# Kernel optimization log

Hardware: AMD Instinct MI355X
Metric: run time of the kernel (lower is better)

## Reference

```python
import jax, jax.numpy as jnp
import numpy as np

N, E = 50000, 800000
IN_DIM, HID, ZDIM = 256, 128, 64
LN_EPS = 1e-5


def _layernorm(x, gamma, beta):
    mu = jnp.mean(x, axis=-1, keepdims=True)
    var = jnp.mean(jnp.square(x - mu), axis=-1, keepdims=True)
    return (x - mu) * jax.lax.rsqrt(var + LN_EPS) * gamma + beta


def _gcn_conv(h, src, dst, dinv, W, b):
    # h: (N, d_in) -> (N, d_out). GCNConv: X W, then sym-normalized
    # aggregation over edges with self-loops, then bias.
    h = h @ W                                   # (N, d_out)
    coef = dinv[src] * dinv[dst]                # (E,)
    agg = jax.ops.segment_sum(h[src] * coef[:, None], dst,
                              num_segments=h.shape[0])
    agg = agg + h * jnp.square(dinv)[:, None]   # self-loop term
    return agg + b


def setup_inputs() -> dict:
    key = jax.random.key(0)
    ks = jax.random.split(key, 5)
    x = jax.random.normal(ks[0], (N, IN_DIM), dtype=jnp.float32)
    edge_index = jax.random.randint(ks[1], (2, E), 0, N, dtype=jnp.int64)
    s1 = 1.0 / np.sqrt(IN_DIM)
    s2 = 1.0 / np.sqrt(HID)
    return {
        "x": x,
        "edge_index": edge_index,
        "ln_gamma": jnp.ones((IN_DIM,), jnp.float32),
        "ln_beta": jnp.zeros((IN_DIM,), jnp.float32),
        "W1": jax.random.normal(ks[2], (IN_DIM, HID), jnp.float32) * s1,
        "b1": jnp.zeros((HID,), jnp.float32),
        "W2": jax.random.normal(ks[3], (HID, HID), jnp.float32) * s2,
        "b2": jnp.zeros((HID,), jnp.float32),
        "W3": jax.random.normal(ks[4], (HID, ZDIM), jnp.float32) * s2,
        "b3": jnp.zeros((ZDIM,), jnp.float32),
    }


def reference(x, edge_index, ln_gamma, ln_beta, W1, b1, W2, b2, W3, b3):
    src, dst = edge_index[0], edge_index[1]
    n = x.shape[0]
    # degree with self-loops (dropout is inference no-op, training=False)
    deg = jnp.ones((n,), x.dtype).at[dst].add(1.0)
    dinv = jax.lax.rsqrt(deg)
    h = _layernorm(x, ln_gamma, ln_beta)
    h = jax.nn.relu(_gcn_conv(h, src, dst, dinv, W1, b1))
    h = jax.nn.relu(_gcn_conv(h, src, dst, dinv, W2, b2))
    z = _gcn_conv(h, src, dst, dinv, W3, b3)
    return z
```

## Files before the change

### kernel.cpp

```cpp
#include <hip/hip_runtime.h>
#include <cstdint>
#include <cstddef>


typedef __attribute__((ext_vector_type(8))) __bf16 bf16x8;
typedef __attribute__((ext_vector_type(4))) float f32x4;
typedef _Float16 half_t;
typedef __attribute__((ext_vector_type(8))) _Float16 half8_t;

#define NHIST 256
#define CHUNK 4096
#define MAXB 8192

__global__ __launch_bounds__(256) void prep_misc(
    const int* __restrict__ dst,
    const float* __restrict__ W1, const float* __restrict__ W2,
    const float* __restrict__ W3,
    int* __restrict__ bcnt_multi,
    unsigned short* __restrict__ W1t_hi, unsigned short* __restrict__ W1t_lo,
    unsigned short* __restrict__ W2t_hi, unsigned short* __restrict__ W2t_lo,
    unsigned short* __restrict__ W3t_hi, unsigned short* __restrict__ W3t_lo,
    int E) {
  int blk = blockIdx.x;
  int tid = threadIdx.x;
  if (blk < NHIST) {
    __shared__ int h[256];
    h[tid] = 0;
    __syncthreads();
    for (int e = blk * 256 + tid; e < E; e += NHIST * 256)
      atomicAdd(&h[dst[e] >> 8], 1);
    __syncthreads();
    bcnt_multi[blk * 256 + tid] = h[tid];
    return;
  }
  int idx = (blk - NHIST) * 256 + tid;
  if (idx < 32768) {
    int k = idx / 128, c = idx % 128;
    float v = W1[idx];
    __bf16 h = (__bf16)v;
    __bf16 l = (__bf16)(v - (float)h);
    W1t_hi[(size_t)c * 256 + k] = __builtin_bit_cast(unsigned short, h);
    W1t_lo[(size_t)c * 256 + k] = __builtin_bit_cast(unsigned short, l);
    return;
  }
  const float* W;
  unsigned short *Th, *Tl;
  int K, NOUT;
  if (idx < 49152) {
    idx -= 32768;
    W = W2; Th = W2t_hi; Tl = W2t_lo; K = 128; NOUT = 128;
  } else {
    idx -= 49152;
    W = W3; Th = W3t_hi; Tl = W3t_lo; K = 128; NOUT = 64;
  }
  int k = idx / NOUT, c = idx % NOUT;
  float v = W[idx];
  half_t h = (half_t)v;
  half_t l = (half_t)((v - (float)h) * 2048.0f);
  Th[(size_t)c * K + k] = __builtin_bit_cast(unsigned short, h);
  Tl[(size_t)c * K + k] = __builtin_bit_cast(unsigned short, l);
}

__global__ __launch_bounds__(256) void scan_buckets(const int* __restrict__ bcnt_multi,
                                                    int* __restrict__ bbase,
                                                    int* __restrict__ bcur, int NB, int E) {
  __shared__ int tmp[256];
  int t = threadIdx.x;
  int v = 0;
  for (int h = 0; h < NHIST; ++h) v += bcnt_multi[h * 256 + t];
  tmp[t] = v;
  __syncthreads();
  for (int off = 1; off < 256; off <<= 1) {
    int x = (t >= off) ? tmp[t - off] : 0;
    __syncthreads();
    tmp[t] += x;
    __syncthreads();
  }
  int excl = tmp[t] - v;
  if (t < NB) { bbase[t] = excl; bcur[t] = excl; }
  if (t == 0) bbase[NB] = E;
}

__device__ __forceinline__ void scatter_body(char* smem_raw, int bid,
                                             const int* __restrict__ src,
                                             const int* __restrict__ dst,
                                             int* __restrict__ bcur,
                                             unsigned int* __restrict__ binned, int E) {
  unsigned int* recs = (unsigned int*)smem_raw;
  int* hist = (int*)(smem_raw + 16384);
  int* lbase = hist + 256;
  int* resv = lbase + 256;
  int* cur = resv + 256;
  int t = threadIdx.x;
  int e0 = bid * CHUNK;
  if (e0 >= E) return;
  int len = min(CHUNK, E - e0);
  hist[t] = 0;
  cur[t] = 0;
  __syncthreads();
  for (int i = t; i < len; i += 256) atomicAdd(&hist[dst[e0 + i] >> 8], 1);
  __syncthreads();
  int v = hist[t];
  lbase[t] = v;
  __syncthreads();
  for (int off = 1; off < 256; off <<= 1) {
    int x = (t >= off) ? lbase[t - off] : 0;
    __syncthreads();
    lbase[t] += x;
    __syncthreads();
  }
  int myexcl = lbase[t] - v;
  if (v) resv[t] = atomicAdd(&bcur[t], v);
  __syncthreads();
  lbase[t] = myexcl;
  __syncthreads();
  for (int i = t; i < len; i += 256) {
    int d = dst[e0 + i], s = src[e0 + i];
    int b = d >> 8;
    int r = atomicAdd(&cur[b], 1);
    recs[lbase[b] + r] = ((unsigned int)d << 16) | (unsigned int)s;
  }
  __syncthreads();
  for (int i = t; i < len; i += 256) {
    unsigned int rc = recs[i];
    int b = rc >> 24;
    binned[resv[b] + (i - lbase[b])] = rc;
  }
}

__device__ __forceinline__ void sort_body(char* smem_raw, int b,
                                          const unsigned int* __restrict__ binned,
                                          const int* __restrict__ bbase,
                                          int* __restrict__ srcs,
                                          int* __restrict__ offs,
                                          float* __restrict__ dinv,
                                          int N, int NB, int E) {
  int* sstage = (int*)smem_raw;
  int* hist = (int*)(smem_raw + 32768);
  int* nbase = hist + 256;
  int* cur = nbase + 256;
  int* tmp = cur + 256;
  int t = threadIdx.x;
  int base = bbase[b], end = bbase[b + 1];
  int L = end - base;
  if (L > MAXB) L = MAXB;
  hist[t] = 0;
  __syncthreads();
  for (int i = t; i < L; i += 256)
    atomicAdd(&hist[(binned[base + i] >> 16) & 255], 1);
  __syncthreads();
  int v = hist[t];
  tmp[t] = v;
  __syncthreads();
  for (int off = 1; off < 256; off <<= 1) {
    int x = (t >= off) ? tmp[t - off] : 0;
    __syncthreads();
    tmp[t] += x;
    __syncthreads();
  }
  int excl = tmp[t] - v;
  nbase[t] = excl;
  cur[t] = excl;
  int node = (b << 8) + t;
  if (node < N) {
    offs[node] = base + excl;
    dinv[node] = rsqrtf(1.0f + (float)v);
  }
  if (b == NB - 1 && t == 0) offs[N] = E;
  __syncthreads();
  for (int i = t; i < L; i += 256) {
    unsigned int p = binned[base + i];
    int ld = (p >> 16) & 255;
    int slot = atomicAdd(&cur[ld], 1);
    sstage[slot] = (int)(p & 0xFFFFu);
  }
  __syncthreads();
  for (int i = t; i < L; i += 256) srcs[base + i] = sstage[i];
}

template <int K, int NOUT, bool LN>
__device__ __forceinline__ void gemm_body(char* smem_raw, int gbid,
                                          const float* __restrict__ A,
                                          const unsigned short* __restrict__ Wt_hi,
                                          const unsigned short* __restrict__ Wt_lo,
                                          const float* __restrict__ gamma,
                                          const float* __restrict__ beta,
                                          half_t* __restrict__ out, int nrows) {
  constexpr int BM = 32, BK = 32, BKP = BK + 8;
  constexpr int NTW = NOUT / 32;

  const int tid = threadIdx.x;
  const int lane = tid & 63;
  const int w = tid >> 6;
  const int quad = lane >> 4;
  const int l16 = lane & 15;
  const int rg = (w & 1) * 16;
  const int cg = (w >> 1) * (NOUT / 2);
  const int row0 = gbid * BM;

  unsigned short* As_hi = (unsigned short*)smem_raw;
  unsigned short* As_lo = As_hi + BM * BKP;
  unsigned short* Bs_hi = As_lo + BM * BKP;
  unsigned short* Bs_lo = Bs_hi + NOUT * BKP;
  float* mu_s = (float*)(Bs_lo + NOUT * BKP);
  float* rs_s = mu_s + BM;

  if constexpr (LN) {
    int r = tid >> 3;
    int part = tid & 7;
    int grow = row0 + r;
    if (grow > nrows - 1) grow = nrows - 1;
    const float4* rp = (const float4*)(A + (size_t)grow * K);
    float s = 0.f, s2 = 0.f;
#pragma unroll
    for (int j = 0; j < K / 32; ++j) {
      float4 v = rp[part * (K / 32) + j];
      s += v.x + v.y + v.z + v.w;
      s2 += v.x * v.x + v.y * v.y + v.z * v.z + v.w * v.w;
    }
    s += __shfl_xor(s, 1);
    s += __shfl_xor(s, 2);
    s += __shfl_xor(s, 4);
    s2 += __shfl_xor(s2, 1);
    s2 += __shfl_xor(s2, 2);
    s2 += __shfl_xor(s2, 4);
    if (part == 0) {
      float m = s * (1.0f / (float)K);
      float var = s2 * (1.0f / (float)K) - m * m;
      mu_s[r] = m;
      rs_s[r] = rsqrtf(var + 1e-5f);
    }
    __syncthreads();
  }

  f32x4 acc[NTW];
#pragma unroll
  for (int t = 0; t < NTW; ++t) acc[t] = (f32x4){0.f, 0.f, 0.f, 0.f};

  for (int k0 = 0; k0 < K; k0 += BK) {
    {
      int r = tid >> 3;
      int c4 = (tid & 7) * 4;
      int grow = row0 + r;
      if (grow > nrows - 1) grow = nrows - 1;
      float4 v = *(const float4*)&A[(size_t)grow * K + k0 + c4];
      if constexpr (LN) {
        float m = mu_s[r], s = rs_s[r];
        float4 g = *(const float4*)&gamma[k0 + c4];
        float4 b = *(const float4*)&beta[k0 + c4];
        v.x = (v.x - m) * s * g.x + b.x;
        v.y = (v.y - m) * s * g.y + b.y;
        v.z = (v.z - m) * s * g.z + b.z;
        v.w = (v.w - m) * s * g.w + b.w;
      }
      float vv[4] = {v.x, v.y, v.z, v.w};
#pragma unroll
      for (int j = 0; j < 4; ++j) {
        __bf16 h = (__bf16)vv[j];
        __bf16 l = (__bf16)(vv[j] - (float)h);
        As_hi[r * BKP + c4 + j] = __builtin_bit_cast(unsigned short, h);
        As_lo[r * BKP + c4 + j] = __builtin_bit_cast(unsigned short, l);
      }
    }
#pragma unroll
    for (int i = 0; i < NOUT / 64; ++i) {
      int n = i * 64 + (tid >> 2);
      int c8 = (tid & 3) * 8;
      *(uint4*)&Bs_hi[n * BKP + c8] = *(const uint4*)&Wt_hi[(size_t)n * K + k0 + c8];
      *(uint4*)&Bs_lo[n * BKP + c8] = *(const uint4*)&Wt_lo[(size_t)n * K + k0 + c8];
    }
    __syncthreads();

    bf16x8 ah = *(const bf16x8*)&As_hi[(rg + l16) * BKP + quad * 8];
    bf16x8 al = *(const bf16x8*)&As_lo[(rg + l16) * BKP + quad * 8];
#pragma unroll
    for (int t = 0; t < NTW; ++t) {
      bf16x8 bh = *(const bf16x8*)&Bs_hi[(cg + t * 16 + l16) * BKP + quad * 8];
      bf16x8 bl = *(const bf16x8*)&Bs_lo[(cg + t * 16 + l16) * BKP + quad * 8];
      acc[t] = __builtin_amdgcn_mfma_f32_16x16x32_bf16(ah, bh, acc[t], 0, 0, 0);
      acc[t] = __builtin_amdgcn_mfma_f32_16x16x32_bf16(al, bh, acc[t], 0, 0, 0);
      acc[t] = __builtin_amdgcn_mfma_f32_16x16x32_bf16(ah, bl, acc[t], 0, 0, 0);
    }
    __syncthreads();
  }

#pragma unroll
  for (int t = 0; t < NTW; ++t) {
#pragma unroll
    for (int r = 0; r < 4; ++r) {
      int grow = row0 + rg + quad * 4 + r;
      if (grow < nrows)
        out[(size_t)grow * NOUT + cg + t * 16 + l16] = (half_t)acc[t][r];
    }
  }
}

constexpr int GEMM1_SMEM = 32 * 40 * 4 + 128 * 40 * 4 + 256;

__global__ __launch_bounds__(256) void fused_scatter_gemm1(
    const int* __restrict__ src, const int* __restrict__ dst,
    int* __restrict__ bcur, unsigned int* __restrict__ binned, int E,
    const float* __restrict__ x,
    const unsigned short* __restrict__ W1t_hi, const unsigned short* __restrict__ W1t_lo,
    const float* __restrict__ gamma, const float* __restrict__ beta,
    half_t* __restrict__ t, int nrows, int nscat) {
  __shared__ __align__(16) char smem[GEMM1_SMEM];
  if ((int)blockIdx.x < nscat)
    scatter_body(smem, blockIdx.x, src, dst, bcur, binned, E);
  else
    gemm_body<256, 128, true>(smem, blockIdx.x - nscat, x, W1t_hi, W1t_lo,
                              gamma, beta, t, nrows);
}

__global__ __launch_bounds__(256) void fused_sort_gemm1(
    const unsigned int* __restrict__ binned, const int* __restrict__ bbase,
    int* __restrict__ srcs, int* __restrict__ offs, float* __restrict__ dinv,
    int N, int NB, int E,
    const float* __restrict__ x,
    const unsigned short* __restrict__ W1t_hi, const unsigned short* __restrict__ W1t_lo,
    const float* __restrict__ gamma, const float* __restrict__ beta,
    half_t* __restrict__ t, int nrows, int g1a) {
  __shared__ __align__(16) char smem[36864];
  if ((int)blockIdx.x < NB)
    sort_body(smem, blockIdx.x, binned, bbase, srcs, offs, dinv, N, NB, E);
  else
    gemm_body<256, 128, true>(smem, g1a + (blockIdx.x - NB), x, W1t_hi, W1t_lo,
                              gamma, beta, t, nrows);
}

template <int NOUT>
__global__ __launch_bounds__(256) void agg_gemm(
    const half_t* __restrict__ tin,
    const int* __restrict__ offs, const int* __restrict__ srcs,
    const float* __restrict__ dinv, const float* __restrict__ bias,
    const unsigned short* __restrict__ Wt_hi,
    const unsigned short* __restrict__ Wt_lo,
    half_t* __restrict__ out, int nrows) {
  constexpr int K = 128, BK = 32, BKP = BK + 8, ROWP = K + 8;
  constexpr int NTW = NOUT / 32;
  __shared__ __align__(16) half_t As[32 * ROWP];
  __shared__ __align__(16) half_t Bs_hi[NOUT * BKP];
  __shared__ __align__(16) half_t Bs_lo[NOUT * BKP];

  const int tid = threadIdx.x;
  const int row0 = blockIdx.x * 32;

  {
    int g = tid >> 4, fl = tid & 15;
#pragma unroll
    for (int rr = g; rr < 32; rr += 16) {
      int node = row0 + rr;
      if (node > nrows - 1) node = nrows - 1;
      int e0 = offs[node], e1 = offs[node + 1];
      float acc[8] = {0.f, 0.f, 0.f, 0.f, 0.f, 0.f, 0.f, 0.f};
      int e = e0;
      for (; e + 3 < e1; e += 4) {
        int sa = srcs[e], sb = srcs[e + 1], sc = srcs[e + 2], sd = srcs[e + 3];
        float wa = dinv[sa], wb = dinv[sb], wc = dinv[sc], wd = dinv[sd];
        half8_t va = *(const half8_t*)(tin + ((size_t)sa << 7) + fl * 8);
        half8_t vb = *(const half8_t*)(tin + ((size_t)sb << 7) + fl * 8);
        half8_t vc = *(const half8_t*)(tin + ((size_t)sc << 7) + fl * 8);
        half8_t vd = *(const half8_t*)(tin + ((size_t)sd << 7) + fl * 8);
#pragma unroll
        for (int j = 0; j < 8; ++j) {
          acc[j] = fmaf(wa, (float)va[j], acc[j]);
          acc[j] = fmaf(wb, (float)vb[j], acc[j]);
          acc[j] = fmaf(wc, (float)vc[j], acc[j]);
          acc[j] = fmaf(wd, (float)vd[j], acc[j]);
        }
      }
      for (; e < e1; ++e) {
        int s = srcs[e];
        float w = dinv[s];
        half8_t v = *(const half8_t*)(tin + ((size_t)s << 7) + fl * 8);
#pragma unroll
        for (int j = 0; j < 8; ++j) acc[j] = fmaf(w, (float)v[j], acc[j]);
      }
      float di = dinv[node];
      float dii = di * di;
      half8_t sv = *(const half8_t*)(tin + ((size_t)node << 7) + fl * 8);
      float4 b0 = *(const float4*)(bias + fl * 8);
      float4 b1 = *(const float4*)(bias + fl * 8 + 4);
      float bb[8] = {b0.x, b0.y, b0.z, b0.w, b1.x, b1.y, b1.z, b1.w};
#pragma unroll
      for (int j = 0; j < 8; ++j) {
        float v = di * acc[j] + dii * (float)sv[j] + bb[j];
        As[rr * ROWP + fl * 8 + j] = (half_t)fmaxf(v, 0.f);
      }
    }
  }
  __syncthreads();

  const int lane = tid & 63;
  const int w = tid >> 6;
  const int quad = lane >> 4;
  const int l16 = lane & 15;
  const int rg = (w & 1) * 16;
  const int cg = (w >> 1) * (NOUT / 2);

  f32x4 acc1[NTW], acc2[NTW];
#pragma unroll
  for (int t = 0; t < NTW; ++t) {
    acc1[t] = (f32x4){0.f, 0.f, 0.f, 0.f};
    acc2[t] = (f32x4){0.f, 0.f, 0.f, 0.f};
  }

  for (int k0 = 0; k0 < K; k0 += BK) {
#pragma unroll
    for (int i = 0; i < NOUT / 64; ++i) {
      int n = i * 64 + (tid >> 2);
      int c8 = (tid & 3) * 8;
      *(uint4*)&Bs_hi[n * BKP + c8] = *(const uint4*)&Wt_hi[(size_t)n * K + k0 + c8];
      *(uint4*)&Bs_lo[n * BKP + c8] = *(const uint4*)&Wt_lo[(size_t)n * K + k0 + c8];
    }
    __syncthreads();

    half8_t av = *(const half8_t*)&As[(rg + l16) * ROWP + k0 + quad * 8];
#pragma unroll
    for (int t = 0; t < NTW; ++t) {
      half8_t bh = *(const half8_t*)&Bs_hi[(cg + t * 16 + l16) * BKP + quad * 8];
      half8_t bl = *(const half8_t*)&Bs_lo[(cg + t * 16 + l16) * BKP + quad * 8];
      acc1[t] = __builtin_amdgcn_mfma_f32_16x16x32_f16(av, bh, acc1[t], 0, 0, 0);
      acc2[t] = __builtin_amdgcn_mfma_f32_16x16x32_f16(av, bl, acc2[t], 0, 0, 0);
    }
    __syncthreads();
  }

#pragma unroll
  for (int t = 0; t < NTW; ++t) {
#pragma unroll
    for (int r = 0; r < 4; ++r) {
      int grow = row0 + rg + quad * 4 + r;
      if (grow < nrows)
        out[(size_t)grow * NOUT + cg + t * 16 + l16] =
            (half_t)(acc1[t][r] + acc2[t][r] * (1.0f / 2048.0f));
    }
  }
}

__global__ __launch_bounds__(256) void agg64_h(const half_t* __restrict__ t,
                                               const int* __restrict__ offs,
                                               const int* __restrict__ srcs,
                                               const float* __restrict__ dinv,
                                               const float* __restrict__ bias,
                                               float* __restrict__ out, int n) {
  int gid = blockIdx.x * blockDim.x + threadIdx.x;
  int node = gid >> 6, lane = gid & 63;
  if (node >= n) return;
  int og = lane >> 3;
  int fl = lane & 7;
  int e0 = offs[node], e1 = offs[node + 1];
  float acc[8] = {0.f, 0.f, 0.f, 0.f, 0.f, 0.f, 0.f, 0.f};
  int e = e0 + og;
  for (; e + 8 < e1; e += 16) {
    int sa = srcs[e], sb = srcs[e + 8];
    float wa = dinv[sa], wb = dinv[sb];
    half8_t va = *(const half8_t*)(t + ((size_t)sa << 6) + fl * 8);
    half8_t vb = *(const half8_t*)(t + ((size_t)sb << 6) + fl * 8);
#pragma unroll
    for (int j = 0; j < 8; ++j) {
      acc[j] = fmaf(wa, (float)va[j], acc[j]);
      acc[j] = fmaf(wb, (float)vb[j], acc[j]);
    }
  }
  for (; e < e1; e += 8) {
    int s = srcs[e];
    float w = dinv[s];
    half8_t v = *(const half8_t*)(t + ((size_t)s << 6) + fl * 8);
#pragma unroll
    for (int j = 0; j < 8; ++j) acc[j] = fmaf(w, (float)v[j], acc[j]);
  }
#pragma unroll
  for (int j = 0; j < 8; ++j) {
    acc[j] += __shfl_xor(acc[j], 8);
    acc[j] += __shfl_xor(acc[j], 16);
    acc[j] += __shfl_xor(acc[j], 32);
  }
  if (og == 0) {
    float di = dinv[node];
    float dii = di * di;
    half8_t sv = *(const half8_t*)(t + ((size_t)node << 6) + fl * 8);
    float4 b0 = *(const float4*)(bias + fl * 8);
    float4 b1 = *(const float4*)(bias + fl * 8 + 4);
    float bb[8] = {b0.x, b0.y, b0.z, b0.w, b1.x, b1.y, b1.z, b1.w};
    float ov[8];
#pragma unroll
    for (int j = 0; j < 8; ++j) ov[j] = di * acc[j] + dii * (float)sv[j] + bb[j];
    *(float4*)(out + ((size_t)node << 6) + fl * 8) = make_float4(ov[0], ov[1], ov[2], ov[3]);
    *(float4*)(out + ((size_t)node << 6) + fl * 8 + 4) = make_float4(ov[4], ov[5], ov[6], ov[7]);
  }
}

extern "C" void kernel_launch(void* const* d_in, const int* in_sizes, int n_in,
                              void* d_out, int out_size, void* d_ws, size_t ws_size,
                              hipStream_t stream) {
  const float* x = (const float*)d_in[0];
  const int* ei = (const int*)d_in[1];
  const float* gamma = (const float*)d_in[2];
  const float* beta = (const float*)d_in[3];
  const float* W1 = (const float*)d_in[4];
  const float* b1 = (const float*)d_in[5];
  const float* W2 = (const float*)d_in[6];
  const float* b2 = (const float*)d_in[7];
  const float* W3 = (const float*)d_in[8];
  const float* b3 = (const float*)d_in[9];
  float* out = (float*)d_out;

  const int N = in_sizes[0] / 256;
  const int E = in_sizes[1] / 2;
  const int* src = ei;
  const int* dst = ei + E;
  const int NB = (N + 255) >> 8;

  char* ws = (char*)d_ws;
  auto alloc = [&](size_t bytes) -> char* {
    char* p = ws;
    ws += (bytes + 255) & ~(size_t)255;
    return p;
  };
  int* bcnt_multi = (int*)alloc(NHIST * 256 * 4);
  int* bbase = (int*)alloc(257 * 4);
  int* bcur = (int*)alloc(256 * 4);
  unsigned int* binned = (unsigned int*)alloc((size_t)E * 4);
  int* srcs = (int*)alloc((size_t)E * 4);
  int* offs = (int*)alloc((size_t)(N + 1) * 4);
  float* dinv = (float*)alloc((size_t)N * 4);
  half_t* t = (half_t*)alloc((size_t)N * 128 * 2);
  half_t* h = (half_t*)alloc((size_t)N * 128 * 2);
  unsigned short* W1t_hi = (unsigned short*)alloc(256 * 128 * 2);
  unsigned short* W1t_lo = (unsigned short*)alloc(256 * 128 * 2);
  unsigned short* W2t_hi = (unsigned short*)alloc(128 * 128 * 2);
  unsigned short* W2t_lo = (unsigned short*)alloc(128 * 128 * 2);
  unsigned short* W3t_hi = (unsigned short*)alloc(128 * 64 * 2);
  unsigned short* W3t_lo = (unsigned short*)alloc(128 * 64 * 2);

  prep_misc<<<NHIST + 224, 256, 0, stream>>>(
      dst, W1, W2, W3, bcnt_multi, W1t_hi, W1t_lo, W2t_hi, W2t_lo,
      W3t_hi, W3t_lo, E);

  scan_buckets<<<1, 256, 0, stream>>>(bcnt_multi, bbase, bcur, NB, E);

  const int gemm_blocks = (N + 31) / 32;
  const int G1A = gemm_blocks / 2;
  const int G1B = gemm_blocks - G1A;
  const int NSCAT = (E + CHUNK - 1) / CHUNK;
  const int agg_blocks = (N + 3) / 4;

  fused_scatter_gemm1<<<NSCAT + G1A, 256, 0, stream>>>(
      src, dst, bcur, binned, E, x, W1t_hi, W1t_lo, gamma, beta, t, N, NSCAT);

  fused_sort_gemm1<<<NB + G1B, 256, 0, stream>>>(
      binned, bbase, srcs, offs, dinv, N, NB, E, x, W1t_hi, W1t_lo, gamma, beta,
      t, N, G1A);

  agg_gemm<128><<<gemm_blocks, 256, 0, stream>>>(
      t, offs, srcs, dinv, b1, W2t_hi, W2t_lo, h, N);

  agg_gemm<64><<<gemm_blocks, 256, 0, stream>>>(
      h, offs, srcs, dinv, b2, W3t_hi, W3t_lo, t, N);

  agg64_h<<<agg_blocks, 256, 0, stream>>>(t, offs, srcs, dinv, b3, out, N);
}
```

Measured before the change: 258.7 us.

## Interleave two-node gathers and read weights directly from global in agg_gemm

The aggregation phase now processes both of each thread group's nodes at once, issuing eight independent row gathers per iteration instead of four, to raise memory-level parallelism. The weight staging through shared memory (with its per-K-step barriers) is removed. The MFMA loop now loads hi/lo weight fragments straight from global/L2 and is fully unrolled. This cuts LDS footprint and syncs, which may raise occupancy, but it increases register pressure and redundant global weight reads across waves.

```diff
diff --git a/kernel.cpp b/kernel.cpp
--- a/kernel.cpp
+++ b/kernel.cpp
@@ -336,56 +336,118 @@
     const unsigned short* __restrict__ Wt_hi,
     const unsigned short* __restrict__ Wt_lo,
     half_t* __restrict__ out, int nrows) {
-  constexpr int K = 128, BK = 32, BKP = BK + 8, ROWP = K + 8;
+  constexpr int K = 128, ROWP = K + 8;
   constexpr int NTW = NOUT / 32;
   __shared__ __align__(16) half_t As[32 * ROWP];
-  __shared__ __align__(16) half_t Bs_hi[NOUT * BKP];
-  __shared__ __align__(16) half_t Bs_lo[NOUT * BKP];
 
   const int tid = threadIdx.x;
   const int row0 = blockIdx.x * 32;
 
   {
-    int g = tid >> 4, fl = tid & 15;
-#pragma unroll
-    for (int rr = g; rr < 32; rr += 16) {
-      int node = row0 + rr;
-      if (node > nrows - 1) node = nrows - 1;
-      int e0 = offs[node], e1 = offs[node + 1];
-      float acc[8] = {0.f, 0.f, 0.f, 0.f, 0.f, 0.f, 0.f, 0.f};
-      int e = e0;
-      for (; e + 3 < e1; e += 4) {
-        int sa = srcs[e], sb = srcs[e + 1], sc = srcs[e + 2], sd = srcs[e + 3];
-        float wa = dinv[sa], wb = dinv[sb], wc = dinv[sc], wd = dinv[sd];
-        half8_t va = *(const half8_t*)(tin + ((size_t)sa << 7) + fl * 8);
-        half8_t vb = *(const half8_t*)(tin + ((size_t)sb << 7) + fl * 8);
-        half8_t vc = *(const half8_t*)(tin + ((size_t)sc << 7) + fl * 8);
-        half8_t vd = *(const half8_t*)(tin + ((size_t)sd << 7) + fl * 8);
-#pragma unroll
-        for (int j = 0; j < 8; ++j) {
-          acc[j] = fmaf(wa, (float)va[j], acc[j]);
-          acc[j] = fmaf(wb, (float)vb[j], acc[j]);
-          acc[j] = fmaf(wc, (float)vc[j], acc[j]);
-          acc[j] = fmaf(wd, (float)vd[j], acc[j]);
-        }
+    const int g = tid >> 4, fl = tid & 15;
+    const half_t* tf = tin + fl * 8;
+    int nA = row0 + g;
+    int nB = row0 + g + 16;
+    if (nA > nrows - 1) nA = nrows - 1;
+    if (nB > nrows - 1) nB = nrows - 1;
+    int a = offs[nA], a1 = offs[nA + 1];
+    int b = offs[nB], b1 = offs[nB + 1];
+    float accA[8] = {0.f, 0.f, 0.f, 0.f, 0.f, 0.f, 0.f, 0.f};
+    float accB[8] = {0.f, 0.f, 0.f, 0.f, 0.f, 0.f, 0.f, 0.f};
+
+    while (a + 3 < a1 && b + 3 < b1) {
+      int sa0 = srcs[a], sa1 = srcs[a + 1], sa2 = srcs[a + 2], sa3 = srcs[a + 3];
+      int sb0 = srcs[b], sb1 = srcs[b + 1], sb2 = srcs[b + 2], sb3 = srcs[b + 3];
+      half8_t vA0 = *(const half8_t*)(tf + ((size_t)sa0 << 7));
+      half8_t vA1 = *(const half8_t*)(tf + ((size_t)sa1 << 7));
+      half8_t vA2 = *(const half8_t*)(tf + ((size_t)sa2 << 7));
+      half8_t vA3 = *(const half8_t*)(tf + ((size_t)sa3 << 7));
+      half8_t vB0 = *(const half8_t*)(tf + ((size_t)sb0 << 7));
+      half8_t vB1 = *(const half8_t*)(tf + ((size_t)sb1 << 7));
+      half8_t vB2 = *(const half8_t*)(tf + ((size_t)sb2 << 7));
+      half8_t vB3 = *(const half8_t*)(tf + ((size_t)sb3 << 7));
+      float wA0 = dinv[sa0], wA1 = dinv[sa1], wA2 = dinv[sa2], wA3 = dinv[sa3];
+      float wB0 = dinv[sb0], wB1 = dinv[sb1], wB2 = dinv[sb2], wB3 = dinv[sb3];
+#pragma unroll
+      for (int j = 0; j < 8; ++j) {
+        accA[j] = fmaf(wA0, (float)vA0[j], accA[j]);
+        accA[j] = fmaf(wA1, (float)vA1[j], accA[j]);
+        accA[j] = fmaf(wA2, (float)vA2[j], accA[j]);
+        accA[j] = fmaf(wA3, (float)vA3[j], accA[j]);
+        accB[j] = fmaf(wB0, (float)vB0[j], accB[j]);
+        accB[j] = fmaf(wB1, (float)vB1[j], accB[j]);
+        accB[j] = fmaf(wB2, (float)vB2[j], accB[j]);
+        accB[j] = fmaf(wB3, (float)vB3[j], accB[j]);
       }
-      for (; e < e1; ++e) {
-        int s = srcs[e];
-        float w = dinv[s];
-        half8_t v = *(const half8_t*)(tin + ((size_t)s << 7) + fl * 8);
-#pragma unroll
-        for (int j = 0; j < 8; ++j) acc[j] = fmaf(w, (float)v[j], acc[j]);
+      a += 4;
+      b += 4;
+    }
+    for (; a + 3 < a1; a += 4) {
+      int s0 = srcs[a], s1 = srcs[a + 1], s2 = srcs[a + 2], s3 = srcs[a + 3];
+      half8_t v0 = *(const half8_t*)(tf + ((size_t)s0 << 7));
+      half8_t v1 = *(const half8_t*)(tf + ((size_t)s1 << 7));
+      half8_t v2 = *(const half8_t*)(tf + ((size_t)s2 << 7));
+      half8_t v3 = *(const half8_t*)(tf + ((size_t)s3 << 7));
+      float w0 = dinv[s0], w1 = dinv[s1], w2 = dinv[s2], w3 = dinv[s3];
+#pragma unroll
+      for (int j = 0; j < 8; ++j) {
+        accA[j] = fmaf(w0, (float)v0[j], accA[j]);
+        accA[j] = fmaf(w1, (float)v1[j], accA[j]);
+        accA[j] = fmaf(w2, (float)v2[j], accA[j]);
+        accA[j] = fmaf(w3, (float)v3[j], accA[j]);
       }
-      float di = dinv[node];
+    }
+    for (; b + 3 < b1; b += 4) {
+      int s0 = srcs[b], s1 = srcs[b + 1], s2 = srcs[b + 2], s3 = srcs[b + 3];
+      half8_t v0 = *(const half8_t*)(tf + ((size_t)s0 << 7));
+      half8_t v1 = *(const half8_t*)(tf + ((size_t)s1 << 7));
+      half8_t v2 = *(const half8_t*)(tf + ((size_t)s2 << 7));
+      half8_t v3 = *(const half8_t*)(tf + ((size_t)s3 << 7));
+      float w0 = dinv[s0], w1 = dinv[s1], w2 = dinv[s2], w3 = dinv[s3];
+#pragma unroll
+      for (int j = 0; j < 8; ++j) {
+        accB[j] = fmaf(w0, (float)v0[j], accB[j]);
+        accB[j] = fmaf(w1, (float)v1[j], accB[j]);
+        accB[j] = fmaf(w2, (float)v2[j], accB[j]);
+        accB[j] = fmaf(w3, (float)v3[j], accB[j]);
+      }
+    }
+    for (; a < a1; ++a) {
+      int s = srcs[a];
+      float w = dinv[s];
+      half8_t v = *(const half8_t*)(tf + ((size_t)s << 7));
+#pragma unroll
+      for (int j = 0; j < 8; ++j) accA[j] = fmaf(w, (float)v[j], accA[j]);
+    }
+    for (; b < b1; ++b) {
+      int s = srcs[b];
+      float w = dinv[s];
+      half8_t v = *(const half8_t*)(tf + ((size_t)s << 7));
+#pragma unroll
+      for (int j = 0; j < 8; ++j) accB[j] = fmaf(w, (float)v[j], accB[j]);
+    }
+
+    float4 b0v = *(const float4*)(bias + fl * 8);
+    float4 b1v = *(const float4*)(bias + fl * 8 + 4);
+    float bb[8] = {b0v.x, b0v.y, b0v.z, b0v.w, b1v.x, b1v.y, b1v.z, b1v.w};
+    {
+      float di = dinv[nA];
       float dii = di * di;
-      half8_t sv = *(const half8_t*)(tin + ((size_t)node << 7) + fl * 8);
-      float4 b0 = *(const float4*)(bias + fl * 8);
-      float4 b1 = *(const float4*)(bias + fl * 8 + 4);
-      float bb[8] = {b0.x, b0.y, b0.z, b0.w, b1.x, b1.y, b1.z, b1.w};
+      half8_t sv = *(const half8_t*)(tf + ((size_t)nA << 7));
 #pragma unroll
       for (int j = 0; j < 8; ++j) {
-        float v = di * acc[j] + dii * (float)sv[j] + bb[j];
-        As[rr * ROWP + fl * 8 + j] = (half_t)fmaxf(v, 0.f);
+        float v = di * accA[j] + dii * (float)sv[j] + bb[j];
+        As[g * ROWP + fl * 8 + j] = (half_t)fmaxf(v, 0.f);
+      }
+    }
+    {
+      float di = dinv[nB];
+      float dii = di * di;
+      half8_t sv = *(const half8_t*)(tf + ((size_t)nB << 7));
+#pragma unroll
+      for (int j = 0; j < 8; ++j) {
+        float v = di * accB[j] + dii * (float)sv[j] + bb[j];
+        As[(g + 16) * ROWP + fl * 8 + j] = (half_t)fmaxf(v, 0.f);
       }
     }
   }
@@ -405,25 +467,17 @@
     acc2[t] = (f32x4){0.f, 0.f, 0.f, 0.f};
   }
 
-  for (int k0 = 0; k0 < K; k0 += BK) {
-#pragma unroll
-    for (int i = 0; i < NOUT / 64; ++i) {
-      int n = i * 64 + (tid >> 2);
-      int c8 = (tid & 3) * 8;
-      *(uint4*)&Bs_hi[n * BKP + c8] = *(const uint4*)&Wt_hi[(size_t)n * K + k0 + c8];
-      *(uint4*)&Bs_lo[n * BKP + c8] = *(const uint4*)&Wt_lo[(size_t)n * K + k0 + c8];
-    }
-    __syncthreads();
-
+#pragma unroll
+  for (int k0 = 0; k0 < K; k0 += 32) {
     half8_t av = *(const half8_t*)&As[(rg + l16) * ROWP + k0 + quad * 8];
 #pragma unroll
     for (int t = 0; t < NTW; ++t) {
-      half8_t bh = *(const half8_t*)&Bs_hi[(cg + t * 16 + l16) * BKP + quad * 8];
-      half8_t bl = *(const half8_t*)&Bs_lo[(cg + t * 16 + l16) * BKP + quad * 8];
+      int n = cg + t * 16 + l16;
+      half8_t bh = *(const half8_t*)&Wt_hi[(size_t)n * K + k0 + quad * 8];
+      half8_t bl = *(const half8_t*)&Wt_lo[(size_t)n * K + k0 + quad * 8];
       acc1[t] = __builtin_amdgcn_mfma_f32_16x16x32_f16(av, bh, acc1[t], 0, 0, 0);
       acc2[t] = __builtin_amdgcn_mfma_f32_16x16x32_f16(av, bl, acc2[t], 0, 0, 0);
     }
-    __syncthreads();
   }
 
 #pragma unroll
```

Result: slower. 292.0 us (+12.9%).
